# Kernel tuning notes

Hardware: AMD Instinct MI355X
Metric: run time of the kernel (lower is better)

Reference implementation:

```python
import jax, jax.numpy as jnp
import numpy as np

B, H, W, C = 4, 64, 64, 256
CK = C // 8  # f/g projection dim = 32


def setup_inputs() -> dict:
    key = jax.random.key(0)
    ks = jax.random.split(key, 4)
    x = jax.random.normal(ks[0], (B, H, W, C), dtype=jnp.float32)
    Wf = jax.random.normal(ks[1], (C, CK), dtype=jnp.float32) * (1.0 / np.sqrt(C))
    Wg = jax.random.normal(ks[2], (C, CK), dtype=jnp.float32) * (1.0 / np.sqrt(C))
    Wh = jax.random.normal(ks[3], (C, C), dtype=jnp.float32) * (1.0 / np.sqrt(C))
    bf = jnp.zeros((CK,), jnp.float32)
    bg = jnp.zeros((CK,), jnp.float32)
    bh = jnp.zeros((C,), jnp.float32)
    return {"x": x, "Wf": Wf, "bf": bf, "Wg": Wg, "bg": bg, "Wh": Wh, "bh": bh}


def reference(x, Wf, bf, Wg, bg, Wh, bh):
    b, h, w, c = x.shape
    n = h * w
    xf = x.reshape(b, n, c)  # 1x1 conv == per-pixel matmul
    f = xf @ Wf + bf         # [b, n, c/8]  (keys)
    g = xf @ Wg + bg         # [b, n, c/8]  (queries)
    hh = xf @ Wh + bh        # [b, n, c]    (values)
    # s[i,j] = g_i . f_j  (tf.matmul(g, f, transpose_b=True))
    s = jnp.einsum('bik,bjk->bij', g, f)
    beta = jax.nn.softmax(s, axis=-1)
    o = jnp.einsum('bij,bjc->bic', beta, hh)
    return x + o.reshape(b, h, w, c)
```

## Files before the change

### kernel.cpp

```cpp
#include <hip/hip_runtime.h>
#include <math.h>

#define CDIM 256
#define CKD  32
#define NPIX 4096
#define BATCH 4
#define NMACRO (NPIX / 64)

typedef __attribute__((ext_vector_type(8)))  short bf16x8;
typedef __attribute__((ext_vector_type(16))) float f32x16;

__device__ inline ushort f2bf(float x) {
    unsigned u = __float_as_uint(x);
    u += 0x7fffu + ((u >> 16) & 1u);
    return (ushort)(u >> 16);
}
__device__ inline unsigned packbf(float a, float b) {
    return (unsigned)f2bf(a) | ((unsigned)f2bf(b) << 16);
}

#define LDS_ASYNC16(gptr, lptr) \
  __builtin_amdgcn_global_load_lds((const __attribute__((address_space(1))) void*)(gptr), \
                                   (__attribute__((address_space(3))) void*)(lptr), 16, 0, 0)

__global__ __launch_bounds__(256) void prep_kernel(
    const float* __restrict__ Wh, const float* __restrict__ Wf,
    const float* __restrict__ Wg, ushort* __restrict__ Wt)
{
    __shared__ float ls[64 * 65];
    const int tid = threadIdx.x;
    const int bid = blockIdx.x;

    if (bid < 16) {
        const int k0 = (bid & 3) * 64, c0 = (bid >> 2) * 64;
        #pragma unroll
        for (int i = 0; i < 16; ++i) {
            int r = i * 4 + (tid >> 6), c = tid & 63;
            ls[r * 65 + c] = Wh[(k0 + r) * 256 + c0 + c];
        }
        __syncthreads();
        #pragma unroll
        for (int i = 0; i < 16; ++i) {
            int cr = i * 4 + (tid >> 6), k = tid & 63;
            Wt[(c0 + cr) * 256 + k0 + k] = f2bf(ls[k * 65 + cr]);
        }
    } else {
        const float* W = (bid == 16) ? Wf : Wg;
        const int rbase = 256 + (bid - 16) * 32;
        #pragma unroll
        for (int kh2 = 0; kh2 < 2; ++kh2) {
            __syncthreads();
            #pragma unroll
            for (int i = 0; i < 16; ++i) {
                int flat = i * 256 + tid;
                int k = flat >> 5, c = flat & 31;
                ls[c * 129 + k] = W[(kh2 * 128 + k) * 32 + c];
            }
            __syncthreads();
            #pragma unroll
            for (int i = 0; i < 16; ++i) {
                int flat = i * 256 + tid;
                int c = flat >> 7, k = flat & 127;
                Wt[(rbase + c) * 256 + kh2 * 128 + k] = f2bf(ls[c * 129 + k]);
            }
        }
    }
}

__global__ __launch_bounds__(256) void proj_kernel(
    const float*  __restrict__ x,
    const ushort* __restrict__ Wt,
    const float*  __restrict__ bfp, const float* __restrict__ bgp,
    const float*  __restrict__ bhp,
    ushort* __restrict__ fo,
    ushort* __restrict__ go,
    ushort* __restrict__ glo,
    ushort* __restrict__ ht)
{
    __shared__ ushort wls[2][1280 * 8];
    __shared__ ushort xls[2][128 * 8];

    const int tid  = threadIdx.x;
    const int w    = tid >> 6;
    const int lane = tid & 63;
    const int hl   = lane >> 5;
    const int ln   = lane & 31;
    const int bid  = blockIdx.x;
    const long long px0 = (long long)bid * 32;
    const int b    = (int)(px0 >> 12);
    const int n0   = (int)(px0 & (NPIX - 1));
    const int kt   = n0 >> 6;
    const int koff = n0 & 63;

    const int sx_px = tid >> 3, sx_j = tid & 7;
    const int sx_o = sx_j >> 1, sx_h = sx_j & 1;
    const int sx_slot = sx_o * 32 + ((sx_px + 2 * sx_o) & 31);

    #pragma unroll
    for (int i = 0; i < 5; ++i) {
        int s = i * 256 + tid;
        int n = s >> 2, o = ((s & 3) - (n >> 1)) & 3;
        LDS_ASYNC16(Wt + n * 256 + o * 8, &wls[0][s * 8]);
    }
    {
        float4 v = *(const float4*)(x + (px0 + sx_px) * CDIM + sx_j * 4);
        uint2 p; p.x = packbf(v.x, v.y); p.y = packbf(v.z, v.w);
        *(uint2*)&xls[0][sx_slot * 8 + sx_h * 4] = p;
    }

    f32x16 acc0={0,0,0,0,0,0,0,0,0,0,0,0,0,0,0,0};
    f32x16 acc1={0,0,0,0,0,0,0,0,0,0,0,0,0,0,0,0};
    f32x16 accfg={0,0,0,0,0,0,0,0,0,0,0,0,0,0,0,0};

    for (int sl = 0; sl < 8; ++sl) {
        const int cur = sl & 1;
        __syncthreads();
        if (sl + 1 < 8) {
            const int nxt = cur ^ 1;
            #pragma unroll
            for (int i = 0; i < 5; ++i) {
                int s = i * 256 + tid;
                int n = s >> 2, o = ((s & 3) - (n >> 1)) & 3;
                LDS_ASYNC16(Wt + n * 256 + (sl + 1) * 32 + o * 8, &wls[nxt][s * 8]);
            }
            float4 v = *(const float4*)(x + (px0 + sx_px) * CDIM + (sl + 1) * 32 + sx_j * 4);
            uint2 p; p.x = packbf(v.x, v.y); p.y = packbf(v.z, v.w);
            *(uint2*)&xls[nxt][sx_slot * 8 + sx_h * 4] = p;
        }

        #pragma unroll
        for (int st = 0; st < 2; ++st) {
            const int o = st * 2 + hl;
            #define LDW(n) (*(const bf16x8*)&wls[cur][((n) * 4 + (((o) + ((n) >> 1)) & 3)) * 8])
            bf16x8 xb  = *(const bf16x8*)&xls[cur][(o * 32 + ((ln + 2 * o) & 31)) * 8];
            bf16x8 wa0 = LDW(w * 64 + ln);
            bf16x8 wa1 = LDW(w * 64 + 32 + ln);
            acc0 = __builtin_amdgcn_mfma_f32_32x32x16_bf16(wa0, xb, acc0, 0, 0, 0);
            acc1 = __builtin_amdgcn_mfma_f32_32x32x16_bf16(wa1, xb, acc1, 0, 0, 0);
            if (w < 2) {
                bf16x8 wfg = LDW(256 + w * 32 + ln);
                accfg = __builtin_amdgcn_mfma_f32_32x32x16_bf16(xb, wfg, accfg, 0, 0, 0);
            }
            #undef LDW
        }
    }

    ushort* htt = ht + ((long long)(b * 64 + kt) * CDIM) * 64 + koff;
    #pragma unroll
    for (int r = 0; r < 16; ++r) {
        const int rowD = (r & 3) + 8 * (r >> 2) + 4 * hl;
        int c0 = w * 64 + rowD, c1 = c0 + 32;
        htt[(long long)c0 * 64 + ln] = f2bf(acc0[r] + bhp[c0]);
        htt[(long long)c1 * 64 + ln] = f2bf(acc1[r] + bhp[c1]);
    }
    if (w < 2) {
        const float bb = (w ? bgp : bfp)[ln];
        #pragma unroll
        for (int r = 0; r < 16; ++r) {
            const int rowD = (r & 3) + 8 * (r >> 2) + 4 * hl;
            float v = accfg[r] + bb;
            ushort hi = f2bf(v);
            long long idx = (px0 + rowD) * CKD + ln;
            if (w == 0) {
                fo[idx] = hi;
            } else {
                go[idx] = hi;
                float hif = __uint_as_float(((unsigned)hi) << 16);
                glo[idx] = f2bf(v - hif);
            }
        }
    }
}

__global__ __launch_bounds__(256, 2) void attn_kernel(
    const float*  __restrict__ x,
    const ushort* __restrict__ fk,
    const ushort* __restrict__ gq,
    const ushort* __restrict__ glo,
    const ushort* __restrict__ hv,
    float* __restrict__ out)
{
    __shared__ ushort hh_lds[2][1024 * 8];
    __shared__ ushort f_lds[2][256 * 8];
    __shared__ float  l_red[2][64];

    const int tid  = threadIdx.x;
    const int w    = tid >> 6;
    const int lane = tid & 63;
    const int hl   = lane >> 5;
    const int ln   = lane & 31;

    const int bid = blockIdx.x;
    const int chs = bid & 1;
    const int b   = (bid >> 1) & 3;
    const int qt  = bid >> 3;
    const int q0  = qt * 64;

    const int qb = w & 1;
    const int kh = w >> 1;

    const long long bbase = (long long)b * NPIX;
    const ushort* fbase = fk + bbase * CKD;
    const ushort* htb   = hv + (long long)b * 64 * (CDIM * 64);

    const ushort* gp  = gq  + (bbase + q0 + qb * 32 + ln) * CKD;
    const ushort* glp = glo + (bbase + q0 + qb * 32 + ln) * CKD;
    const bf16x8 ga0 = *(const bf16x8*)(gp + hl * 8);
    const bf16x8 ga1 = *(const bf16x8*)(gp + 16 + hl * 8);
    const bf16x8 gl0 = *(const bf16x8*)(glp + hl * 8);
    const bf16x8 gl1 = *(const bf16x8*)(glp + 16 + hl * 8);

    #pragma unroll
    for (int i = 0; i < 4; ++i) {
        int s = i * 256 + tid;
        int c = s >> 3, j = ((s & 7) - c) & 7;
        LDS_ASYNC16(htb + (long long)(chs * 128 + c) * 64 + j * 8, &hh_lds[0][s * 8]);
    }
    LDS_ASYNC16(fbase + (long long)(tid & 63) * CKD + (tid >> 6) * 8, &f_lds[0][tid * 8]);

    f32x16 acc0={0,0,0,0,0,0,0,0,0,0,0,0,0,0,0,0};
    f32x16 acc1={0,0,0,0,0,0,0,0,0,0,0,0,0,0,0,0};
    f32x16 acc2={0,0,0,0,0,0,0,0,0,0,0,0,0,0,0,0};
    f32x16 acc3={0,0,0,0,0,0,0,0,0,0,0,0,0,0,0,0};
    float lsum = 0.f;

    for (int kt = 0; kt < NMACRO; ++kt) {
        const int cur = kt & 1;
        __syncthreads();

        if (kt + 1 < NMACRO) {
            const int nxt = cur ^ 1;
            const long long tb = (long long)(kt + 1) * (CDIM * 64);
            #pragma unroll
            for (int i = 0; i < 4; ++i) {
                int s = i * 256 + tid;
                int c = s >> 3, j = ((s & 7) - c) & 7;
                LDS_ASYNC16(htb + tb + (long long)(chs * 128 + c) * 64 + j * 8,
                            &hh_lds[nxt][s * 8]);
            }
            LDS_ASYNC16(fbase + (long long)((kt + 1) * 64 + (tid & 63)) * CKD + (tid >> 6) * 8,
                        &f_lds[nxt][tid * 8]);
        }

        f32x16 S={0,0,0,0,0,0,0,0,0,0,0,0,0,0,0,0};
        {
            bf16x8 fb0 = *(const bf16x8*)&f_lds[cur][((hl)     * 64 + kh * 32 + ln) * 8];
            bf16x8 fb1 = *(const bf16x8*)&f_lds[cur][((2 + hl) * 64 + kh * 32 + ln) * 8];
            S = __builtin_amdgcn_mfma_f32_32x32x16_bf16(fb0, ga0, S, 0, 0, 0);
            S = __builtin_amdgcn_mfma_f32_32x32x16_bf16(fb0, gl0, S, 0, 0, 0);
            S = __builtin_amdgcn_mfma_f32_32x32x16_bf16(fb1, ga1, S, 0, 0, 0);
            S = __builtin_amdgcn_mfma_f32_32x32x16_bf16(fb1, gl1, S, 0, 0, 0);
        }

        float p[16];
        #pragma unroll
        for (int r = 0; r < 16; ++r) {
            p[r] = __expf(fminf(S[r], 80.f));
            lsum += p[r];
        }
        unsigned U[8];
        #pragma unroll
        for (int m = 0; m < 8; ++m) U[m] = packbf(p[2*m], p[2*m+1]);

        #pragma unroll
        for (int ck = 0; ck < 2; ++ck) {
            unsigned vx = hl ? U[4*ck]     : U[4*ck + 2];
            unsigned vy = hl ? U[4*ck + 1] : U[4*ck + 3];
            unsigned rx = (unsigned)__shfl_xor((int)vx, 32);
            unsigned ry = (unsigned)__shfl_xor((int)vy, 32);
            union { unsigned i[4]; bf16x8 v; } pf;
            pf.i[0] = hl ? rx : U[4*ck];
            pf.i[1] = hl ? ry : U[4*ck + 1];
            pf.i[2] = hl ? U[4*ck + 2] : rx;
            pf.i[3] = hl ? U[4*ck + 3] : ry;
            bf16x8 pa = pf.v;
            const int oct = kh * 4 + ck * 2 + hl;
            const int c0 = ln, c1 = 32 + ln, c2 = 64 + ln, c3 = 96 + ln;
            bf16x8 hb0 = *(const bf16x8*)&hh_lds[cur][(c0 * 8 + ((oct + c0) & 7)) * 8];
            bf16x8 hb1 = *(const bf16x8*)&hh_lds[cur][(c1 * 8 + ((oct + c1) & 7)) * 8];
            bf16x8 hb2 = *(const bf16x8*)&hh_lds[cur][(c2 * 8 + ((oct + c2) & 7)) * 8];
            bf16x8 hb3 = *(const bf16x8*)&hh_lds[cur][(c3 * 8 + ((oct + c3) & 7)) * 8];
            acc0 = __builtin_amdgcn_mfma_f32_32x32x16_bf16(pa, hb0, acc0, 0, 0, 0);
            acc1 = __builtin_amdgcn_mfma_f32_32x32x16_bf16(pa, hb1, acc1, 0, 0, 0);
            acc2 = __builtin_amdgcn_mfma_f32_32x32x16_bf16(pa, hb2, acc2, 0, 0, 0);
            acc3 = __builtin_amdgcn_mfma_f32_32x32x16_bf16(pa, hb3, acc3, 0, 0, 0);
        }
    }

    lsum += __shfl_xor(lsum, 32);
    __syncthreads();
    if (hl == 0) l_red[kh][qb * 32 + ln] = lsum;
    float* O_s = (float*)hh_lds;
    if (kh == 0) {
        #pragma unroll
        for (int r = 0; r < 16; ++r) {
            int rowD = (r & 3) + 8 * (r >> 2) + 4 * hl;
            O_s[((qb * 4 + 2) * 32 + rowD) * 32 + ln] = acc2[r];
            O_s[((qb * 4 + 3) * 32 + rowD) * 32 + ln] = acc3[r];
        }
    } else {
        #pragma unroll
        for (int r = 0; r < 16; ++r) {
            int rowD = (r & 3) + 8 * (r >> 2) + 4 * hl;
            O_s[((qb * 4 + 0) * 32 + rowD) * 32 + ln] = acc0[r];
            O_s[((qb * 4 + 1) * 32 + rowD) * 32 + ln] = acc1[r];
        }
    }
    __syncthreads();

    if (kh == 0) {
        #pragma unroll
        for (int r = 0; r < 16; ++r) {
            int rowD = (r & 3) + 8 * (r >> 2) + 4 * hl;
            int ql = qb * 32 + rowD;
            float linv = 1.f / (l_red[0][ql] + l_red[1][ql]);
            long long rg = (bbase + q0 + ql) * CDIM + chs * 128 + ln;
            float o0 = acc0[r] + O_s[((qb * 4 + 0) * 32 + rowD) * 32 + ln];
            float o1 = acc1[r] + O_s[((qb * 4 + 1) * 32 + rowD) * 32 + ln];
            out[rg]      = x[rg]      + o0 * linv;
            out[rg + 32] = x[rg + 32] + o1 * linv;
        }
    } else {
        #pragma unroll
        for (int r = 0; r < 16; ++r) {
            int rowD = (r & 3) + 8 * (r >> 2) + 4 * hl;
            int ql = qb * 32 + rowD;
            float linv = 1.f / (l_red[0][ql] + l_red[1][ql]);
            long long rg = (bbase + q0 + ql) * CDIM + chs * 128 + 64 + ln;
            float o2 = acc2[r] + O_s[((qb * 4 + 2) * 32 + rowD) * 32 + ln];
            float o3 = acc3[r] + O_s[((qb * 4 + 3) * 32 + rowD) * 32 + ln];
            out[rg]      = x[rg]      + o2 * linv;
            out[rg + 32] = x[rg + 32] + o3 * linv;
        }
    }
}

extern "C" void kernel_launch(void* const* d_in, const int* in_sizes, int n_in,
                              void* d_out, int out_size, void* d_ws, size_t ws_size,
                              hipStream_t stream) {
    const float* x  = (const float*)d_in[0];
    const float* Wf = (const float*)d_in[1];
    const float* bf = (const float*)d_in[2];
    const float* Wg = (const float*)d_in[3];
    const float* bg = (const float*)d_in[4];
    const float* Wh = (const float*)d_in[5];
    const float* bh = (const float*)d_in[6];
    float* out = (float*)d_out;

    ushort* fbf = (ushort*)d_ws;
    ushort* gbf = fbf + BATCH * NPIX * CKD;
    ushort* glo = gbf + BATCH * NPIX * CKD;
    ushort* ht  = glo + BATCH * NPIX * CKD;
    ushort* Wt  = ht + BATCH * NPIX * CDIM;

    prep_kernel<<<dim3(18), 256, 0, stream>>>(Wh, Wf, Wg, Wt);
    proj_kernel<<<dim3(512), 256, 0, stream>>>(x, Wt, bf, bg, bh, fbf, gbf, glo, ht);
    attn_kernel<<<dim3(512), 256, 0, stream>>>(x, fbf, gbf, glo, ht, out);
}
```

Measured before the change: 163.9 us.

## Use hardware bf16 pack, exp2 with pre-scaled queries, permlane swap and MFMA priority

Replaces the software bf16 round-and-pack with the v_cvt_pk_bf16_f32 instruction. Folds log2(e) into the query projection so the softmax can use a native exp2. Replaces the two shfl_xor exchanges and selects with v_permlane32_swap. It also seeds the score MFMA from a zero constant, wraps the MFMA groups in s_setprio, and unrolls the key loop by two. Together these cut VALU and cross-lane work in the attention inner loop, at the cost of small rounding differences from scaling g before the bf16 hi/lo split.

Result: no change. 162.3 us (-1.0%).

```diff
diff --git a/kernel.cpp b/kernel.cpp
--- a/kernel.cpp
+++ b/kernel.cpp
@@ -10,13 +10,24 @@
 typedef __attribute__((ext_vector_type(8)))  short bf16x8;
 typedef __attribute__((ext_vector_type(16))) float f32x16;
 
+#if __has_builtin(__builtin_amdgcn_exp2f)
+#define EXP2(x) __builtin_amdgcn_exp2f(x)
+#else
+#define EXP2(x) exp2f(x)
+#endif
+
 __device__ inline ushort f2bf(float x) {
     unsigned u = __float_as_uint(x);
     u += 0x7fffu + ((u >> 16) & 1u);
     return (ushort)(u >> 16);
 }
-__device__ inline unsigned packbf(float a, float b) {
-    return (unsigned)f2bf(a) | ((unsigned)f2bf(b) << 16);
+__device__ inline unsigned cvtpk(float a, float b) {
+    unsigned r;
+    asm("v_cvt_pk_bf16_f32 %0, %1, %2" : "=v"(r) : "v"(a), "v"(b));
+    return r;
+}
+__device__ inline void lane32swap(unsigned &a, unsigned &b) {
+    asm("v_permlane32_swap_b32 %0, %1" : "+v"(a), "+v"(b));
 }
 
 #define LDS_ASYNC16(gptr, lptr) \
@@ -104,7 +115,7 @@
     }
     {
         float4 v = *(const float4*)(x + (px0 + sx_px) * CDIM + sx_j * 4);
-        uint2 p; p.x = packbf(v.x, v.y); p.y = packbf(v.z, v.w);
+        uint2 p; p.x = cvtpk(v.x, v.y); p.y = cvtpk(v.z, v.w);
         *(uint2*)&xls[0][sx_slot * 8 + sx_h * 4] = p;
     }
 
@@ -124,7 +135,7 @@
                 LDS_ASYNC16(Wt + n * 256 + (sl + 1) * 32 + o * 8, &wls[nxt][s * 8]);
             }
             float4 v = *(const float4*)(x + (px0 + sx_px) * CDIM + (sl + 1) * 32 + sx_j * 4);
-            uint2 p; p.x = packbf(v.x, v.y); p.y = packbf(v.z, v.w);
+            uint2 p; p.x = cvtpk(v.x, v.y); p.y = cvtpk(v.z, v.w);
             *(uint2*)&xls[nxt][sx_slot * 8 + sx_h * 4] = p;
         }
 
@@ -155,10 +166,11 @@
     }
     if (w < 2) {
         const float bb = (w ? bgp : bfp)[ln];
+        const float scl = w ? 1.44269504088896f : 1.0f;
         #pragma unroll
         for (int r = 0; r < 16; ++r) {
             const int rowD = (r & 3) + 8 * (r >> 2) + 4 * hl;
-            float v = accfg[r] + bb;
+            float v = (accfg[r] + bb) * scl;
             ushort hi = f2bf(v);
             long long idx = (px0 + rowD) * CKD + ln;
             if (w == 0) {
@@ -218,12 +230,14 @@
     }
     LDS_ASYNC16(fbase + (long long)(tid & 63) * CKD + (tid >> 6) * 8, &f_lds[0][tid * 8]);
 
+    const f32x16 Zv = {0,0,0,0,0,0,0,0,0,0,0,0,0,0,0,0};
     f32x16 acc0={0,0,0,0,0,0,0,0,0,0,0,0,0,0,0,0};
     f32x16 acc1={0,0,0,0,0,0,0,0,0,0,0,0,0,0,0,0};
     f32x16 acc2={0,0,0,0,0,0,0,0,0,0,0,0,0,0,0,0};
     f32x16 acc3={0,0,0,0,0,0,0,0,0,0,0,0,0,0,0,0};
     float lsum = 0.f;
 
+    #pragma unroll 2
     for (int kt = 0; kt < NMACRO; ++kt) {
         const int cur = kt & 1;
         __syncthreads();
@@ -242,37 +256,36 @@
                         &f_lds[nxt][tid * 8]);
         }
 
-        f32x16 S={0,0,0,0,0,0,0,0,0,0,0,0,0,0,0,0};
+        f32x16 S;
         {
             bf16x8 fb0 = *(const bf16x8*)&f_lds[cur][((hl)     * 64 + kh * 32 + ln) * 8];
             bf16x8 fb1 = *(const bf16x8*)&f_lds[cur][((2 + hl) * 64 + kh * 32 + ln) * 8];
-            S = __builtin_amdgcn_mfma_f32_32x32x16_bf16(fb0, ga0, S, 0, 0, 0);
+            __builtin_amdgcn_s_setprio(1);
+            S = __builtin_amdgcn_mfma_f32_32x32x16_bf16(fb0, ga0, Zv, 0, 0, 0);
             S = __builtin_amdgcn_mfma_f32_32x32x16_bf16(fb0, gl0, S, 0, 0, 0);
             S = __builtin_amdgcn_mfma_f32_32x32x16_bf16(fb1, ga1, S, 0, 0, 0);
             S = __builtin_amdgcn_mfma_f32_32x32x16_bf16(fb1, gl1, S, 0, 0, 0);
+            __builtin_amdgcn_s_setprio(0);
         }
 
         float p[16];
         #pragma unroll
         for (int r = 0; r < 16; ++r) {
-            p[r] = __expf(fminf(S[r], 80.f));
+            p[r] = EXP2(fminf(S[r], 115.41f));
             lsum += p[r];
         }
         unsigned U[8];
         #pragma unroll
-        for (int m = 0; m < 8; ++m) U[m] = packbf(p[2*m], p[2*m+1]);
+        for (int m = 0; m < 8; ++m) U[m] = cvtpk(p[2*m], p[2*m+1]);
 
         #pragma unroll
         for (int ck = 0; ck < 2; ++ck) {
-            unsigned vx = hl ? U[4*ck]     : U[4*ck + 2];
-            unsigned vy = hl ? U[4*ck + 1] : U[4*ck + 3];
-            unsigned rx = (unsigned)__shfl_xor((int)vx, 32);
-            unsigned ry = (unsigned)__shfl_xor((int)vy, 32);
+            unsigned a0 = U[4*ck + 0], a1 = U[4*ck + 1];
+            unsigned a2 = U[4*ck + 2], a3 = U[4*ck + 3];
+            lane32swap(a0, a2);
+            lane32swap(a1, a3);
             union { unsigned i[4]; bf16x8 v; } pf;
-            pf.i[0] = hl ? rx : U[4*ck];
-            pf.i[1] = hl ? ry : U[4*ck + 1];
-            pf.i[2] = hl ? U[4*ck + 2] : rx;
-            pf.i[3] = hl ? U[4*ck + 3] : ry;
+            pf.i[0] = a0; pf.i[1] = a1; pf.i[2] = a2; pf.i[3] = a3;
             bf16x8 pa = pf.v;
             const int oct = kh * 4 + ck * 2 + hl;
             const int c0 = ln, c1 = 32 + ln, c2 = 64 + ln, c3 = 96 + ln;
@@ -280,10 +293,12 @@
             bf16x8 hb1 = *(const bf16x8*)&hh_lds[cur][(c1 * 8 + ((oct + c1) & 7)) * 8];
             bf16x8 hb2 = *(const bf16x8*)&hh_lds[cur][(c2 * 8 + ((oct + c2) & 7)) * 8];
             bf16x8 hb3 = *(const bf16x8*)&hh_lds[cur][(c3 * 8 + ((oct + c3) & 7)) * 8];
+            __builtin_amdgcn_s_setprio(1);
             acc0 = __builtin_amdgcn_mfma_f32_32x32x16_bf16(pa, hb0, acc0, 0, 0, 0);
             acc1 = __builtin_amdgcn_mfma_f32_32x32x16_bf16(pa, hb1, acc1, 0, 0, 0);
             acc2 = __builtin_amdgcn_mfma_f32_32x32x16_bf16(pa, hb2, acc2, 0, 0, 0);
             acc3 = __builtin_amdgcn_mfma_f32_32x32x16_bf16(pa, hb3, acc3, 0, 0, 0);
+            __builtin_amdgcn_s_setprio(0);
         }
     }
 
```
